# Kernel tuning notes

Measured on AMD Instinct MI355X. Metric: run time of the kernel, lower is better.

## Reference

```python
import jax, jax.numpy as jnp
import numpy as np

S = 4096
F = 512  # in_features, head_num == 1 so per-head dim == F


def setup_inputs() -> dict:
    key = jax.random.key(0)
    ks = jax.random.split(key, 11)
    std = 0.02
    inp = {
        "q": jax.random.normal(ks[0], (1, S, F), jnp.float32),
        "k": jax.random.normal(ks[1], (1, S, F), jnp.float32),
        "v": jax.random.normal(ks[2], (1, S, F), jnp.float32),
        "Wq": jax.random.normal(ks[3], (F, F), jnp.float32) * std,
        "bq": jax.random.normal(ks[4], (F,), jnp.float32) * std,
        "Wk": jax.random.normal(ks[5], (F, F), jnp.float32) * std,
        "bk": jax.random.normal(ks[6], (F,), jnp.float32) * std,
        "Wv": jax.random.normal(ks[7], (F, F), jnp.float32) * std,
        "bv": jax.random.normal(ks[8], (F,), jnp.float32) * std,
        "Wo": jax.random.normal(ks[9], (F, F), jnp.float32) * std,
        "bo": jax.random.normal(ks[10], (F,), jnp.float32) * std,
    }
    return inp


def reference(q, k, v, Wq, bq, Wk, bk, Wv, bv, Wo, bo):
    dk = Wq.shape[0]  # head_num == 1 -> per-head dim equals in_features
    # q_k, q_v: projections of q WITHOUT activation (as in original forward)
    q_k = q @ Wk.T + bk            # (1, S, F)
    q_v = q @ Wv.T + bv            # (1, S, F)
    # activated projections (F.relu)
    qq = jax.nn.relu(q @ Wq.T + bq)[0]  # (S, F)
    kk = jax.nn.relu(k @ Wk.T + bk)[0]  # (S, F)
    vv = jax.nn.relu(v @ Wv.T + bv)[0]  # (S, F)
    # diagonal of qq @ q_k^T, computed without materializing the SxS matrix
    q_att = jnp.sum(qq * q_k[0], axis=-1, keepdims=True)  # (S, 1)
    scores = jnp.einsum('sd,td->st', qq, kk)               # (S, S)
    scores = jnp.concatenate([scores, q_att], axis=-1)     # (S, S+1)
    scores = scores / np.sqrt(dk + 1).astype(np.float32)
    attn = jax.nn.softmax(scores, axis=-1)                 # (S, S+1)
    res = attn[:, :-1] @ vv                                # (S, F)
    res = q_v[0] * q_att + res                             # elementwise fusion
    y = res[None]                                          # (1, S, F)
    y = jax.nn.relu(y @ Wo.T + bo)
    return y
```

## Files before the change

kernel.cpp:

```cpp
#include <hip/hip_runtime.h>
#include <math.h>

#define S_LEN 4096
#define F_DIM 512
#define PSPLIT 4
#define FIXED_M 4.0f

typedef __attribute__((ext_vector_type(8))) short bf16x8;
typedef __attribute__((ext_vector_type(4))) float f32x4;

__device__ __forceinline__ unsigned short f2bf(float x) {
    union { float f; unsigned u; } v; v.f = x;
    unsigned r = v.u + 0x7fffu + ((v.u >> 16) & 1u);
    return (unsigned short)(r >> 16);
}
__device__ __forceinline__ float bf2f(unsigned short b) {
    union { unsigned u; float f; } v; v.u = ((unsigned)b) << 16;
    return v.f;
}
__device__ __forceinline__ void load_lds16(const void* g, void* l) {
    __builtin_amdgcn_global_load_lds(
        (const __attribute__((address_space(1))) unsigned int*)g,
        (__attribute__((address_space(3))) unsigned int*)l, 16, 0, 0);
}

struct CastArgs {
    const float* src[7];
    unsigned short* dst[7];
    int n4[7];
};
__global__ void cast_all(CastArgs a) {
    int r = blockIdx.y;
    int i = blockIdx.x * blockDim.x + threadIdx.x;
    if (i >= a.n4[r]) return;
    float4 v = ((const float4*)a.src[r])[i];
    ushort4 o;
    o.x = f2bf(v.x); o.y = f2bf(v.y); o.z = f2bf(v.z); o.w = f2bf(v.w);
    ((ushort4*)a.dst[r])[i] = o;
}

__global__ void transpose_bf16(const unsigned short* __restrict__ src,
                               unsigned short* __restrict__ dst) {
    __shared__ __align__(16) unsigned short tile[64][72];
    const int s0 = blockIdx.x * 64, f0 = blockIdx.y * 64;
    const int tid = threadIdx.x;
#pragma unroll
    for (int it = 0; it < 2; ++it) {
        int u = it * 256 + tid;
        int r = u >> 3, c = (u & 7) * 8;
        *(uint4*)&tile[r][c] = *(const uint4*)(src + (size_t)(s0 + r) * F_DIM + f0 + c);
    }
    __syncthreads();
#pragma unroll
    for (int it = 0; it < 2; ++it) {
        int u = it * 256 + tid;
        int fl = u >> 3, sc = (u & 7) * 8;
        unsigned short tmp[8];
#pragma unroll
        for (int i = 0; i < 8; ++i) tmp[i] = tile[sc + i][fl];
        *(uint4*)(dst + (size_t)(f0 + fl) * S_LEN + s0 + sc) = *(uint4*)tmp;
    }
}

struct GemmDesc {
    const unsigned short* X;
    const unsigned short* W;
    const float* bias;
    unsigned short* out_bf;
    float* out_f32;
    int relu;
};
struct GemmArgs { GemmDesc d[5]; };

__launch_bounds__(256, 2)
__global__ void gemm128(GemmArgs args) {
    __shared__ __align__(16) unsigned short As[8 * 512];
    __shared__ __align__(16) unsigned short Bs[8 * 512];
    const GemmDesc d = args.d[blockIdx.y >> 2];
    const int n0 = (blockIdx.y & 3) * 128;
    const int m0 = blockIdx.x * 128;
    const int tid = threadIdx.x;
    const int w = tid >> 6, l = tid & 63, quad = l >> 4, ln = l & 15;
    const int wr = w >> 1, wc = w & 1;

    f32x4 acc[4][4];
    f32x4 zero4 = {0.f, 0.f, 0.f, 0.f};
#pragma unroll
    for (int i = 0; i < 4; ++i)
#pragma unroll
        for (int j = 0; j < 4; ++j) acc[i][j] = zero4;

    for (int k0 = 0; k0 < F_DIM; k0 += 32) {
        __syncthreads();
#pragma unroll
        for (int i = 0; i < 2; ++i) {
            int c = w * 2 + i;
            load_lds16(d.X + (size_t)(m0 + c * 16 + ln) * F_DIM + k0 + quad * 8, &As[c * 512]);
            load_lds16(d.W + (size_t)(n0 + c * 16 + ln) * F_DIM + k0 + quad * 8, &Bs[c * 512]);
        }
        __syncthreads();
        bf16x8 af[4], bfr[4];
#pragma unroll
        for (int mt = 0; mt < 4; ++mt)
            af[mt] = *(const bf16x8*)&As[(wr * 4 + mt) * 512 + l * 8];
#pragma unroll
        for (int nt = 0; nt < 4; ++nt)
            bfr[nt] = *(const bf16x8*)&Bs[(wc * 4 + nt) * 512 + l * 8];
#pragma unroll
        for (int mt = 0; mt < 4; ++mt)
#pragma unroll
            for (int nt = 0; nt < 4; ++nt)
                acc[mt][nt] = __builtin_amdgcn_mfma_f32_16x16x32_bf16(af[mt], bfr[nt], acc[mt][nt], 0, 0, 0);
    }

#pragma unroll
    for (int mt = 0; mt < 4; ++mt)
#pragma unroll
        for (int nt = 0; nt < 4; ++nt)
#pragma unroll
            for (int r = 0; r < 4; ++r) {
                int row = m0 + wr * 64 + mt * 16 + quad * 4 + r;
                int col = n0 + wc * 64 + nt * 16 + ln;
                float vv = acc[mt][nt][r] + d.bias[col];
                if (d.relu) vv = fmaxf(vv, 0.f);
                if (d.out_bf)  d.out_bf[(size_t)row * F_DIM + col] = f2bf(vv);
                if (d.out_f32) d.out_f32[(size_t)row * F_DIM + col] = vv;
            }
}

__launch_bounds__(256, 2)
__global__ void gemm_exp(const unsigned short* __restrict__ X,
                         const unsigned short* __restrict__ W,
                         unsigned short* __restrict__ P,
                         float* __restrict__ lpart) {
    __shared__ __align__(16) unsigned short As[8 * 512];
    __shared__ __align__(16) unsigned short Bs[8 * 512];
    __shared__ float lsum[2][2][64];
    const float scale = 0.04415108f;
    const int nb = blockIdx.y;
    const int n0 = nb * 128;
    const int m0 = blockIdx.x * 128;
    const int tid = threadIdx.x;
    const int w = tid >> 6, l = tid & 63, quad = l >> 4, ln = l & 15;
    const int wr = w >> 1, wc = w & 1;

    f32x4 acc[4][4];
    f32x4 zero4 = {0.f, 0.f, 0.f, 0.f};
#pragma unroll
    for (int i = 0; i < 4; ++i)
#pragma unroll
        for (int j = 0; j < 4; ++j) acc[i][j] = zero4;

    for (int k0 = 0; k0 < F_DIM; k0 += 32) {
        __syncthreads();
#pragma unroll
        for (int i = 0; i < 2; ++i) {
            int c = w * 2 + i;
            load_lds16(X + (size_t)(m0 + c * 16 + ln) * F_DIM + k0 + quad * 8, &As[c * 512]);
            load_lds16(W + (size_t)(n0 + c * 16 + ln) * F_DIM + k0 + quad * 8, &Bs[c * 512]);
        }
        __syncthreads();
        bf16x8 af[4], bfr[4];
#pragma unroll
        for (int mt = 0; mt < 4; ++mt)
            af[mt] = *(const bf16x8*)&As[(wr * 4 + mt) * 512 + l * 8];
#pragma unroll
        for (int nt = 0; nt < 4; ++nt)
            bfr[nt] = *(const bf16x8*)&Bs[(wc * 4 + nt) * 512 + l * 8];
#pragma unroll
        for (int mt = 0; mt < 4; ++mt)
#pragma unroll
            for (int nt = 0; nt < 4; ++nt)
                acc[mt][nt] = __builtin_amdgcn_mfma_f32_16x16x32_bf16(af[mt], bfr[nt], acc[mt][nt], 0, 0, 0);
    }

    float rs[4][4];
#pragma unroll
    for (int mt = 0; mt < 4; ++mt)
#pragma unroll
        for (int r = 0; r < 4; ++r) rs[mt][r] = 0.f;

#pragma unroll
    for (int mt = 0; mt < 4; ++mt)
#pragma unroll
        for (int nt = 0; nt < 4; ++nt)
#pragma unroll
            for (int r = 0; r < 4; ++r) {
                int row = m0 + wr * 64 + mt * 16 + quad * 4 + r;
                int col = n0 + wc * 64 + nt * 16 + ln;
                float p = __expf(acc[mt][nt][r] * scale - FIXED_M);
                P[(size_t)row * S_LEN + col] = f2bf(p);
                rs[mt][r] += p;
            }
#pragma unroll
    for (int mt = 0; mt < 4; ++mt)
#pragma unroll
        for (int r = 0; r < 4; ++r) {
            float v = rs[mt][r];
            v += __shfl_xor(v, 1);
            v += __shfl_xor(v, 2);
            v += __shfl_xor(v, 4);
            v += __shfl_xor(v, 8);
            if (ln == 0) lsum[wr][wc][mt * 16 + quad * 4 + r] = v;
        }
    __syncthreads();
    if (tid < 128)
        lpart[(size_t)nb * S_LEN + m0 + tid] =
            lsum[tid >> 6][0][tid & 63] + lsum[tid >> 6][1][tid & 63];
}

__launch_bounds__(256, 2)
__global__ void gemm_pv(const unsigned short* __restrict__ P,
                        const unsigned short* __restrict__ vt,
                        float* __restrict__ O_p) {
    __shared__ __align__(16) unsigned short As[8 * 512];
    __shared__ __align__(16) unsigned short Bs[8 * 512];
    const int nb = blockIdx.y & 3;
    const int split = blockIdx.y >> 2;
    const int n0 = nb * 128;
    const int m0 = blockIdx.x * 128;
    const int koff = split * (S_LEN / PSPLIT);
    const int tid = threadIdx.x;
    const int w = tid >> 6, l = tid & 63, quad = l >> 4, ln = l & 15;
    const int wr = w >> 1, wc = w & 1;

    f32x4 acc[4][4];
    f32x4 zero4 = {0.f, 0.f, 0.f, 0.f};
#pragma unroll
    for (int i = 0; i < 4; ++i)
#pragma unroll
        for (int j = 0; j < 4; ++j) acc[i][j] = zero4;

    for (int k0 = koff; k0 < koff + S_LEN / PSPLIT; k0 += 32) {
        __syncthreads();
#pragma unroll
        for (int i = 0; i < 2; ++i) {
            int c = w * 2 + i;
            load_lds16(P + (size_t)(m0 + c * 16 + ln) * S_LEN + k0 + quad * 8, &As[c * 512]);
            load_lds16(vt + (size_t)(n0 + c * 16 + ln) * S_LEN + k0 + quad * 8, &Bs[c * 512]);
        }
        __syncthreads();
        bf16x8 af[4], bfr[4];
#pragma unroll
        for (int mt = 0; mt < 4; ++mt)
            af[mt] = *(const bf16x8*)&As[(wr * 4 + mt) * 512 + l * 8];
#pragma unroll
        for (int nt = 0; nt < 4; ++nt)
            bfr[nt] = *(const bf16x8*)&Bs[(wc * 4 + nt) * 512 + l * 8];
#pragma unroll
        for (int mt = 0; mt < 4; ++mt)
#pragma unroll
            for (int nt = 0; nt < 4; ++nt)
                acc[mt][nt] = __builtin_amdgcn_mfma_f32_16x16x32_bf16(af[mt], bfr[nt], acc[mt][nt], 0, 0, 0);
    }

    float* Op = O_p + (size_t)split * S_LEN * F_DIM;
#pragma unroll
    for (int mt = 0; mt < 4; ++mt)
#pragma unroll
        for (int nt = 0; nt < 4; ++nt)
#pragma unroll
            for (int r = 0; r < 4; ++r) {
                int row = m0 + wr * 64 + mt * 16 + quad * 4 + r;
                int col = n0 + wc * 64 + nt * 16 + ln;
                Op[(size_t)row * F_DIM + col] = acc[mt][nt][r];
            }
}

__global__ void combine_kernel(const float* __restrict__ O_p,
                               const float* __restrict__ lpart,
                               const unsigned short* __restrict__ qq,
                               const unsigned short* __restrict__ qk,
                               const unsigned short* __restrict__ qv,
                               unsigned short* __restrict__ res_bf) {
    const float scale = 0.04415108f;
    int row = blockIdx.x;
    int t = threadIdx.x;
    int wv = t >> 6, l = t & 63;
    __shared__ float wsum[2];

    ushort4 a = *(const ushort4*)(qq + (size_t)row * F_DIM + t * 4);
    ushort4 b = *(const ushort4*)(qk + (size_t)row * F_DIM + t * 4);
    float part = bf2f(a.x) * bf2f(b.x) + bf2f(a.y) * bf2f(b.y) +
                 bf2f(a.z) * bf2f(b.z) + bf2f(a.w) * bf2f(b.w);
#pragma unroll
    for (int off = 32; off >= 1; off >>= 1) part += __shfl_xor(part, off);
    if (l == 0) wsum[wv] = part;
    __syncthreads();
    float qa = wsum[0] + wsum[1];

    float denom = __expf(qa * scale - FIXED_M);
#pragma unroll
    for (int i = 0; i < 32; ++i) denom += lpart[(size_t)i * S_LEN + row];
    float inv = 1.f / denom;

    for (int f = t; f < F_DIM; f += 128) {
        float acc = 0.f;
#pragma unroll
        for (int i = 0; i < PSPLIT; ++i)
            acc += O_p[((size_t)i * S_LEN + row) * F_DIM + f];
        float r = bf2f(qv[(size_t)row * F_DIM + f]) * qa + acc * inv;
        res_bf[(size_t)row * F_DIM + f] = f2bf(r);
    }
}

extern "C" void kernel_launch(void* const* d_in, const int* in_sizes, int n_in,
                              void* d_out, int out_size, void* d_ws, size_t ws_size,
                              hipStream_t stream) {
    const float* q  = (const float*)d_in[0];
    const float* k  = (const float*)d_in[1];
    const float* v  = (const float*)d_in[2];
    const float* Wq = (const float*)d_in[3];
    const float* bq = (const float*)d_in[4];
    const float* Wk = (const float*)d_in[5];
    const float* bk = (const float*)d_in[6];
    const float* Wv = (const float*)d_in[7];
    const float* bv = (const float*)d_in[8];
    const float* Wo = (const float*)d_in[9];
    const float* bo = (const float*)d_in[10];
    float* out = (float*)d_out;

    char* p = (char*)d_ws;
    auto alloc = [&](size_t bytes) -> char* {
        char* r = p; p += (bytes + 255) & ~(size_t)255; return r;
    };
    const size_t SF = (size_t)S_LEN * F_DIM;
    unsigned short* q_bf  = (unsigned short*)alloc(SF * 2);
    unsigned short* k_bf  = (unsigned short*)alloc(SF * 2);
    unsigned short* v_bf  = (unsigned short*)alloc(SF * 2);
    unsigned short* qq_bf = (unsigned short*)alloc(SF * 2);
    unsigned short* kk_bf = (unsigned short*)alloc(SF * 2);
    unsigned short* vv_bf = (unsigned short*)alloc(SF * 2);
    unsigned short* vt_bf = (unsigned short*)alloc(SF * 2);
    unsigned short* qk_bf = (unsigned short*)alloc(SF * 2);
    unsigned short* qv_bf = (unsigned short*)alloc(SF * 2);
    unsigned short* res_bf = (unsigned short*)alloc(SF * 2);
    unsigned short* wq_bf = (unsigned short*)alloc((size_t)F_DIM * F_DIM * 2);
    unsigned short* wk_bf = (unsigned short*)alloc((size_t)F_DIM * F_DIM * 2);
    unsigned short* wv_bf = (unsigned short*)alloc((size_t)F_DIM * F_DIM * 2);
    unsigned short* wo_bf = (unsigned short*)alloc((size_t)F_DIM * F_DIM * 2);
    unsigned short* P_bf  = (unsigned short*)alloc((size_t)S_LEN * S_LEN * 2);
    float* lpart = (float*)alloc((size_t)32 * S_LEN * 4);
    float* O_p   = (float*)alloc((size_t)PSPLIT * SF * 4);

    CastArgs ca;
    ca.src[0] = q;  ca.dst[0] = q_bf;  ca.n4[0] = (int)(SF / 4);
    ca.src[1] = k;  ca.dst[1] = k_bf;  ca.n4[1] = (int)(SF / 4);
    ca.src[2] = v;  ca.dst[2] = v_bf;  ca.n4[2] = (int)(SF / 4);
    ca.src[3] = Wq; ca.dst[3] = wq_bf; ca.n4[3] = F_DIM * F_DIM / 4;
    ca.src[4] = Wk; ca.dst[4] = wk_bf; ca.n4[4] = F_DIM * F_DIM / 4;
    ca.src[5] = Wv; ca.dst[5] = wv_bf; ca.n4[5] = F_DIM * F_DIM / 4;
    ca.src[6] = Wo; ca.dst[6] = wo_bf; ca.n4[6] = F_DIM * F_DIM / 4;
    cast_all<<<dim3((unsigned)(SF / 4 / 256), 7), 256, 0, stream>>>(ca);

    GemmArgs ga;
    ga.d[0] = { q_bf, wq_bf, bq, qq_bf, nullptr, 1 };
    ga.d[1] = { k_bf, wk_bf, bk, kk_bf, nullptr, 1 };
    ga.d[2] = { v_bf, wv_bf, bv, vv_bf, nullptr, 1 };
    ga.d[3] = { q_bf, wk_bf, bk, qk_bf, nullptr, 0 };
    ga.d[4] = { q_bf, wv_bf, bv, qv_bf, nullptr, 0 };
    gemm128<<<dim3(S_LEN / 128, 20), 256, 0, stream>>>(ga);

    transpose_bf16<<<dim3(S_LEN / 64, F_DIM / 64), 256, 0, stream>>>(vv_bf, vt_bf);

    gemm_exp<<<dim3(S_LEN / 128, S_LEN / 128), 256, 0, stream>>>(qq_bf, kk_bf, P_bf, lpart);

    gemm_pv<<<dim3(S_LEN / 128, 4 * PSPLIT), 256, 0, stream>>>(P_bf, vt_bf, O_p);

    combine_kernel<<<S_LEN, 128, 0, stream>>>(O_p, lpart, qq_bf, qk_bf, qv_bf, res_bf);

    GemmArgs ga2{};
    ga2.d[0] = { res_bf, wo_bf, bo, nullptr, out, 1 };
    gemm128<<<dim3(S_LEN / 128, 4), 256, 0, stream>>>(ga2);
}
```

Before: 242.8 us.

## Double K-step per barrier, raise PV split-K to 8, store partials in bf16

Replaces the three GEMM K-loops with a shared macro that loads a 64-wide K slice per pair of barriers instead of 32, which halves barrier count and doubles LDS per block. The PV GEMM split-K factor rises from 4 to 8 to give more blocks (more parallelism), and its partial outputs are written as bf16 instead of fp32 to cut workspace traffic in the combine step. The trade-offs are lower precision in the partial sums, more partials to read in combine, and higher LDS use that may affect occupancy.

```diff
diff --git a/kernel.cpp b/kernel.cpp
--- a/kernel.cpp
+++ b/kernel.cpp
@@ -3,7 +3,7 @@
 
 #define S_LEN 4096
 #define F_DIM 512
-#define PSPLIT 4
+#define PSPLIT 8
 #define FIXED_M 4.0f
 
 typedef __attribute__((ext_vector_type(8))) short bf16x8;
@@ -62,6 +62,39 @@
     }
 }
 
+#define GEMM_KLOOP(XPTR, LDX, WPTR, LDW, KBEG, KEND)                                  \
+    for (int k0 = (KBEG); k0 < (KEND); k0 += 64) {                                    \
+        __syncthreads();                                                              \
+        _Pragma("unroll")                                                             \
+        for (int i = 0; i < 2; ++i) {                                                 \
+            int c = w * 2 + i;                                                        \
+            _Pragma("unroll")                                                         \
+            for (int kh = 0; kh < 2; ++kh) {                                          \
+                load_lds16((XPTR) + (size_t)(m0 + c * 16 + ln) * (LDX) + k0 + kh * 32 + quad * 8, \
+                           &As[(c * 2 + kh) * 512]);                                  \
+                load_lds16((WPTR) + (size_t)(n0 + c * 16 + ln) * (LDW) + k0 + kh * 32 + quad * 8, \
+                           &Bs[(c * 2 + kh) * 512]);                                  \
+            }                                                                         \
+        }                                                                             \
+        __syncthreads();                                                              \
+        _Pragma("unroll")                                                             \
+        for (int kh = 0; kh < 2; ++kh) {                                              \
+            bf16x8 af[4], bfr[4];                                                     \
+            _Pragma("unroll")                                                         \
+            for (int mt = 0; mt < 4; ++mt)                                            \
+                af[mt] = *(const bf16x8*)&As[((wr * 4 + mt) * 2 + kh) * 512 + l * 8];  \
+            _Pragma("unroll")                                                         \
+            for (int nt = 0; nt < 4; ++nt)                                            \
+                bfr[nt] = *(const bf16x8*)&Bs[((wc * 4 + nt) * 2 + kh) * 512 + l * 8]; \
+            _Pragma("unroll")                                                         \
+            for (int mt = 0; mt < 4; ++mt)                                            \
+                _Pragma("unroll")                                                     \
+                for (int nt = 0; nt < 4; ++nt)                                        \
+                    acc[mt][nt] = __builtin_amdgcn_mfma_f32_16x16x32_bf16(            \
+                        af[mt], bfr[nt], acc[mt][nt], 0, 0, 0);                       \
+        }                                                                             \
+    }
+
 struct GemmDesc {
     const unsigned short* X;
     const unsigned short* W;
@@ -74,8 +107,8 @@
 
 __launch_bounds__(256, 2)
 __global__ void gemm128(GemmArgs args) {
-    __shared__ __align__(16) unsigned short As[8 * 512];
-    __shared__ __align__(16) unsigned short Bs[8 * 512];
+    __shared__ __align__(16) unsigned short As[16 * 512];
+    __shared__ __align__(16) unsigned short Bs[16 * 512];
     const GemmDesc d = args.d[blockIdx.y >> 2];
     const int n0 = (blockIdx.y & 3) * 128;
     const int m0 = blockIdx.x * 128;
@@ -90,28 +123,7 @@
 #pragma unroll
         for (int j = 0; j < 4; ++j) acc[i][j] = zero4;
 
-    for (int k0 = 0; k0 < F_DIM; k0 += 32) {
-        __syncthreads();
-#pragma unroll
-        for (int i = 0; i < 2; ++i) {
-            int c = w * 2 + i;
-            load_lds16(d.X + (size_t)(m0 + c * 16 + ln) * F_DIM + k0 + quad * 8, &As[c * 512]);
-            load_lds16(d.W + (size_t)(n0 + c * 16 + ln) * F_DIM + k0 + quad * 8, &Bs[c * 512]);
-        }
-        __syncthreads();
-        bf16x8 af[4], bfr[4];
-#pragma unroll
-        for (int mt = 0; mt < 4; ++mt)
-            af[mt] = *(const bf16x8*)&As[(wr * 4 + mt) * 512 + l * 8];
-#pragma unroll
-        for (int nt = 0; nt < 4; ++nt)
-            bfr[nt] = *(const bf16x8*)&Bs[(wc * 4 + nt) * 512 + l * 8];
-#pragma unroll
-        for (int mt = 0; mt < 4; ++mt)
-#pragma unroll
-            for (int nt = 0; nt < 4; ++nt)
-                acc[mt][nt] = __builtin_amdgcn_mfma_f32_16x16x32_bf16(af[mt], bfr[nt], acc[mt][nt], 0, 0, 0);
-    }
+    GEMM_KLOOP(d.X, F_DIM, d.W, F_DIM, 0, F_DIM)
 
 #pragma unroll
     for (int mt = 0; mt < 4; ++mt)
@@ -133,8 +145,8 @@
                          const unsigned short* __restrict__ W,
                          unsigned short* __restrict__ P,
                          float* __restrict__ lpart) {
-    __shared__ __align__(16) unsigned short As[8 * 512];
-    __shared__ __align__(16) unsigned short Bs[8 * 512];
+    __shared__ __align__(16) unsigned short As[16 * 512];
+    __shared__ __align__(16) unsigned short Bs[16 * 512];
     __shared__ float lsum[2][2][64];
     const float scale = 0.04415108f;
     const int nb = blockIdx.y;
@@ -151,28 +163,7 @@
 #pragma unroll
         for (int j = 0; j < 4; ++j) acc[i][j] = zero4;
 
-    for (int k0 = 0; k0 < F_DIM; k0 += 32) {
-        __syncthreads();
-#pragma unroll
-        for (int i = 0; i < 2; ++i) {
-            int c = w * 2 + i;
-            load_lds16(X + (size_t)(m0 + c * 16 + ln) * F_DIM + k0 + quad * 8, &As[c * 512]);
-            load_lds16(W + (size_t)(n0 + c * 16 + ln) * F_DIM + k0 + quad * 8, &Bs[c * 512]);
-        }
-        __syncthreads();
-        bf16x8 af[4], bfr[4];
-#pragma unroll
-        for (int mt = 0; mt < 4; ++mt)
-            af[mt] = *(const bf16x8*)&As[(wr * 4 + mt) * 512 + l * 8];
-#pragma unroll
-        for (int nt = 0; nt < 4; ++nt)
-            bfr[nt] = *(const bf16x8*)&Bs[(wc * 4 + nt) * 512 + l * 8];
-#pragma unroll
-        for (int mt = 0; mt < 4; ++mt)
-#pragma unroll
-            for (int nt = 0; nt < 4; ++nt)
-                acc[mt][nt] = __builtin_amdgcn_mfma_f32_16x16x32_bf16(af[mt], bfr[nt], acc[mt][nt], 0, 0, 0);
-    }
+    GEMM_KLOOP(X, F_DIM, W, F_DIM, 0, F_DIM)
 
     float rs[4][4];
 #pragma unroll
@@ -212,9 +203,9 @@
 __launch_bounds__(256, 2)
 __global__ void gemm_pv(const unsigned short* __restrict__ P,
                         const unsigned short* __restrict__ vt,
-                        float* __restrict__ O_p) {
-    __shared__ __align__(16) unsigned short As[8 * 512];
-    __shared__ __align__(16) unsigned short Bs[8 * 512];
+                        unsigned short* __restrict__ O_p) {
+    __shared__ __align__(16) unsigned short As[16 * 512];
+    __shared__ __align__(16) unsigned short Bs[16 * 512];
     const int nb = blockIdx.y & 3;
     const int split = blockIdx.y >> 2;
     const int n0 = nb * 128;
@@ -231,30 +222,9 @@
 #pragma unroll
         for (int j = 0; j < 4; ++j) acc[i][j] = zero4;
 
-    for (int k0 = koff; k0 < koff + S_LEN / PSPLIT; k0 += 32) {
-        __syncthreads();
-#pragma unroll
-        for (int i = 0; i < 2; ++i) {
-            int c = w * 2 + i;
-            load_lds16(P + (size_t)(m0 + c * 16 + ln) * S_LEN + k0 + quad * 8, &As[c * 512]);
-            load_lds16(vt + (size_t)(n0 + c * 16 + ln) * S_LEN + k0 + quad * 8, &Bs[c * 512]);
-        }
-        __syncthreads();
-        bf16x8 af[4], bfr[4];
-#pragma unroll
-        for (int mt = 0; mt < 4; ++mt)
-            af[mt] = *(const bf16x8*)&As[(wr * 4 + mt) * 512 + l * 8];
-#pragma unroll
-        for (int nt = 0; nt < 4; ++nt)
-            bfr[nt] = *(const bf16x8*)&Bs[(wc * 4 + nt) * 512 + l * 8];
-#pragma unroll
-        for (int mt = 0; mt < 4; ++mt)
-#pragma unroll
-            for (int nt = 0; nt < 4; ++nt)
-                acc[mt][nt] = __builtin_amdgcn_mfma_f32_16x16x32_bf16(af[mt], bfr[nt], acc[mt][nt], 0, 0, 0);
-    }
-
-    float* Op = O_p + (size_t)split * S_LEN * F_DIM;
+    GEMM_KLOOP(P, S_LEN, vt, S_LEN, koff, koff + S_LEN / PSPLIT)
+
+    unsigned short* Op = O_p + (size_t)split * S_LEN * F_DIM;
 #pragma unroll
     for (int mt = 0; mt < 4; ++mt)
 #pragma unroll
@@ -263,11 +233,11 @@
             for (int r = 0; r < 4; ++r) {
                 int row = m0 + wr * 64 + mt * 16 + quad * 4 + r;
                 int col = n0 + wc * 64 + nt * 16 + ln;
-                Op[(size_t)row * F_DIM + col] = acc[mt][nt][r];
+                Op[(size_t)row * F_DIM + col] = f2bf(acc[mt][nt][r]);
             }
 }
 
-__global__ void combine_kernel(const float* __restrict__ O_p,
+__global__ void combine_kernel(const unsigned short* __restrict__ O_p,
                                const float* __restrict__ lpart,
                                const unsigned short* __restrict__ qq,
                                const unsigned short* __restrict__ qk,
@@ -298,7 +268,7 @@
         float acc = 0.f;
 #pragma unroll
         for (int i = 0; i < PSPLIT; ++i)
-            acc += O_p[((size_t)i * S_LEN + row) * F_DIM + f];
+            acc += bf2f(O_p[((size_t)i * S_LEN + row) * F_DIM + f]);
         float r = bf2f(qv[(size_t)row * F_DIM + f]) * qa + acc * inv;
         res_bf[(size_t)row * F_DIM + f] = f2bf(r);
     }
@@ -341,7 +311,7 @@
     unsigned short* wo_bf = (unsigned short*)alloc((size_t)F_DIM * F_DIM * 2);
     unsigned short* P_bf  = (unsigned short*)alloc((size_t)S_LEN * S_LEN * 2);
     float* lpart = (float*)alloc((size_t)32 * S_LEN * 4);
-    float* O_p   = (float*)alloc((size_t)PSPLIT * SF * 4);
+    unsigned short* O_p = (unsigned short*)alloc((size_t)PSPLIT * SF * 2);
 
     CastArgs ca;
     ca.src[0] = q;  ca.dst[0] = q_bf;  ca.n4[0] = (int)(SF / 4);
```

New measurement: 245.3 us. About the same (+1.0%).
